# Kernel optimization log

Hardware: AMD Instinct MI355X
Metric: run time of the kernel (lower is better)

## Reference

```python
import math
import jax, jax.numpy as jnp
import numpy as np

MAX_CH = 21
D_CONV = 1024
LAT_DIM = 5
N_HEADS = 2            # TST_encoder hard-codes n_heads=2 (not PatchTSTEncoder's n_heads=8)
D_FF = 256
L_RAW = 38400
CONV_SPECS = [(512, 10, 5, 1), (512, 3, 2, 1), (512, 3, 2, 1), (1024, 3, 2, 1)]  # (dim,k,stride,dilation)
T_FRAMES = 959         # ((((38400-10)//5+1 -3)//2+1 -3)//2+1 -3)//2+1
T_TOTAL = MAX_CH * T_FRAMES  # 20139
L_LAT = MAX_CH * LAT_DIM     # 105


def sinusoid_table(n, d):
    pos = jnp.arange(n, dtype=jnp.float32)[:, None]
    div = jnp.exp(jnp.arange(0, d, 2, dtype=jnp.float32) * (-math.log(10000.0) / d))
    pe = jnp.zeros((n, d), jnp.float32)
    pe = pe.at[:, 0::2].set(jnp.sin(pos * div))
    pe = pe.at[:, 1::2].set(jnp.cos(pos * div))
    return pe


def setup_inputs() -> dict:
    key = jax.random.key(0)
    ks = jax.random.split(key, 16)
    x = jax.random.normal(ks[0], (1, MAX_CH, L_RAW), dtype=jnp.float32)
    # per-channel validity mask: first 17 of 21 channels valid, broadcast over frames
    ch_valid = jnp.arange(MAX_CH) < 17
    ch_mask = jnp.repeat(ch_valid, T_FRAMES)[None, None, :]  # (1,1,T_TOTAL) bool

    conv_params = {}
    in_c = 1
    for i, (dim, k, s, dil) in enumerate(CONV_SPECS):
        std = 1.0 / math.sqrt(in_c * k)
        conv_params[f"conv_w{i+1}"] = jax.random.normal(ks[1 + i], (dim, in_c, k), jnp.float32) * std
        conv_params[f"conv_b{i+1}"] = jnp.zeros((dim,), jnp.float32)
        in_c = dim

    ch_emb = sinusoid_table(MAX_CH, D_CONV)  # trainable channel embedding, sinusoidal init
    latent_q = jax.random.normal(ks[6], (L_LAT, D_CONV), jnp.float32) * math.sqrt(2.0 / (L_LAT + D_CONV))
    std_d = 1.0 / math.sqrt(D_CONV)
    wk_w = jax.random.normal(ks[7], (D_CONV, D_CONV), jnp.float32) * std_d
    wk_b = jnp.zeros((D_CONV,), jnp.float32)
    wv_w = jax.random.normal(ks[8], (D_CONV, D_CONV), jnp.float32) * std_d
    wv_b = jnp.zeros((D_CONV,), jnp.float32)
    ff_w1 = jax.random.normal(ks[9], (D_FF, D_CONV), jnp.float32) * std_d   # Linear(d_conv->d_ff), no bias
    ff_w2 = jax.random.normal(ks[10], (D_CONV, D_FF), jnp.float32) * (1.0 / math.sqrt(D_FF))
    return dict(x=x,
                conv_w1=conv_params["conv_w1"], conv_b1=conv_params["conv_b1"],
                conv_w2=conv_params["conv_w2"], conv_b2=conv_params["conv_b2"],
                conv_w3=conv_params["conv_w3"], conv_b3=conv_params["conv_b3"],
                conv_w4=conv_params["conv_w4"], conv_b4=conv_params["conv_b4"],
                ch_emb=ch_emb, latent_q=latent_q,
                wk_w=wk_w, wk_b=wk_b, wv_w=wv_w, wv_b=wv_b,
                ff_w1=ff_w1, ff_w2=ff_w2, ch_mask=ch_mask)


def _conv1d(x, w, b, stride, dilation):
    # x: (N, C_in, L), w: (C_out, C_in, K)
    y = jax.lax.conv_general_dilated(x, w, window_strides=(stride,), padding='VALID',
                                     rhs_dilation=(dilation,),
                                     dimension_numbers=('NCH', 'OIH', 'NCH'))
    return y + b[None, :, None]


def reference(x, conv_w1, conv_b1, conv_w2, conv_b2, conv_w3, conv_b3, conv_w4, conv_b4,
              ch_emb, latent_q, wk_w, wk_b, wv_w, wv_b, ff_w1, ff_w2, ch_mask):
    b, c_in, L = x.shape
    # --- ConvFeatureExtraction: per-channel conv stack (dropout is identity at eval) ---
    h = x.reshape(b * c_in, 1, L)
    weights = [(conv_w1, conv_b1), (conv_w2, conv_b2), (conv_w3, conv_b3), (conv_w4, conv_b4)]
    for (w, bi), (_, k, s, dil) in zip(weights, CONV_SPECS):
        h = jax.nn.gelu(_conv1d(h, w, bi, s, dil), approximate=False)
    t = h.shape[-1]
    x_conv = h.reshape(b, c_in, D_CONV, t).transpose(0, 1, 3, 2)  # (b, c_in, t, d_conv)

    # --- DataEmbedding: temporal sinusoid (buffer) + channel embedding (param) ---
    pe = sinusoid_table(t, D_CONV)                                # (t, d_conv)
    x_pos = x_conv + pe[None, None] + ch_emb[None, :, None, :]
    u = x_pos.reshape(b, c_in * t, D_CONV)                        # (1, T, d_conv)

    # --- perceiver_resampler (pre_norm=False: no LayerNorms applied) ---
    T = u.shape[1]
    d_h = D_CONV // N_HEADS
    lq = latent_q.reshape(1, N_HEADS, L_LAT, d_h)                 # exact torch .view semantics
    kproj = (u @ wk_w.T + wk_b).reshape(b, T, N_HEADS, d_h)
    vproj = (u @ wv_w.T + wv_b).reshape(b, T, N_HEADS, d_h)
    k = kproj.transpose(0, 2, 3, 1)                               # (b, H, d, T)
    v = vproj.transpose(0, 2, 1, 3)                               # (b, H, T, d)
    scale = N_HEADS ** (-0.5)                                     # note: heads, not d_k
    scores = jnp.einsum('bhld,bhdt->bhlt', lq, k) * scale         # (b, H, L_lat, T)
    mask = ch_mask[:, None, :, :]                                 # (b,1,1,T) -> broadcast
    scores = jnp.where(mask, scores, -1000000000.0)
    attn = jax.nn.softmax(scores, axis=-1)
    attn = jnp.where(mask, attn, 0.0)
    o = jnp.einsum('bhlt,bhtd->bhld', attn, v)                    # (b, H, L_lat, d)
    o = o.transpose(0, 2, 1, 3).reshape(b, L_LAT, D_CONV)

    # --- GELU FFN (bias=False) + residual ---
    ffn = jax.nn.gelu(o @ ff_w1.T, approximate=False) @ ff_w2.T
    return o + ffn
```

## Files before the change

### kernel.cpp

```cpp
#include <hip/hip_runtime.h>
#include <math.h>


#define NCH 17
#define LRAW 38400
#define LC1 7679
#define LC2 3839
#define LC3 1919
#define LC4 959
#define XA1 3840
#define XA2 1920
#define XA3 960
#define DC 1024
#define TVALID (NCH * LC4)
#define TPAD 16320
#define LLAT 105
#define DH 512
#define ASTR 40
#define ESTR 132

typedef unsigned short u16;
typedef __attribute__((ext_vector_type(8))) short bf16x8;
typedef __attribute__((ext_vector_type(4))) float f32x4;

__device__ __forceinline__ float bf2f(u16 s) {
    union { unsigned int u; float f; } cv; cv.u = ((unsigned int)s) << 16; return cv.f;
}
__device__ __forceinline__ u16 f2bf(float f) {
    union { float f; unsigned int u; } cv; cv.f = f;
    unsigned int u = cv.u;
    u += 0x7FFFu + ((u >> 16) & 1u);
    return (u16)(u >> 16);
}
__device__ __forceinline__ float gelu_exact(float x) {
    return 0.5f * x * (1.0f + erff(x * 0.70710678118654752f));
}
__device__ __forceinline__ float gelu_fast(float x) {
    float u = 0.7978845608f * x * (1.0f + 0.044715f * x * x);
    u = fminf(fmaxf(u, -9.0f), 9.0f);
    float e = __expf(2.0f * u);
    return 0.5f * x * (1.0f + (e - 1.0f) / (e + 1.0f));
}

__device__ __forceinline__ void gload16(const u16* g, u16* l) {
    __builtin_amdgcn_global_load_lds(
        (const __attribute__((address_space(1))) void*)g,
        (__attribute__((address_space(3))) void*)l, 16, 0, 0);
}

__device__ __forceinline__ int xcd_logical(int d, int N) {
    int q = N >> 3, r = N & 7, x = d & 7, j = d >> 3;
    return (x < r ? x * (q + 1) : r * (q + 1) + (x - r) * q) + j;
}

#define STAGE_TILE(lds, src, row0, ld, k0)                                          \
    {                                                                               \
        int m_ = tid >> 2, c_ = tid & 3;                                            \
        gload16(&(src)[(size_t)((row0) + m_) * (ld) + (k0) + ((c_ ^ ((m_ >> 1) & 3)) << 3)], \
                &(lds)[m_ * 32 + c_ * 8]);                                          \
        int m2_ = m_ + 64;                                                          \
        gload16(&(src)[(size_t)((row0) + m2_) * (ld) + (k0) + ((c_ ^ ((m2_ >> 1) & 3)) << 3)], \
                &(lds)[m2_ * 32 + c_ * 8]);                                         \
    }

#define FRAG(lds, R) \
    (*reinterpret_cast<const bf16x8*>(&(lds)[(R) * 32 + ((l4 ^ (((R) >> 1) & 3)) << 3)]))

__global__ void __launch_bounds__(256) cvt_kernel(
        const float* __restrict__ in, u16* __restrict__ out, int n) {
    int i = blockIdx.x * 256 + threadIdx.x;
    if (i < n) out[i] = f2bf(in[i]);
}

__global__ void __launch_bounds__(256) wsplit_kernel(
        const float* __restrict__ w, u16* __restrict__ out, int dout) {
    int idx = blockIdx.x * 256 + threadIdx.x;
    if (idx >= dout * 1536) return;
    int d = idx / 1536, k = idx - d * 1536;
    int ci = k / 3, jj = k - ci * 3;
    out[((size_t)jj * dout + d) * 512 + ci] = f2bf(w[idx]);
}

__global__ void __launch_bounds__(256) lqcvt_kernel(
        const float* __restrict__ lq, u16* __restrict__ lqbf) {
    int idx = blockIdx.x * 256 + threadIdx.x;
    if (idx >= 2 * 128 * 512) return;
    int h = idx >> 16, rem = idx & 65535;
    int m = rem >> 9, k = rem & 511;
    lqbf[idx] = (m < LLAT) ? f2bf(lq[(size_t)h * LLAT * DH + m * DH + k]) : (u16)0;
}

__global__ void __launch_bounds__(256) pe_kernel(float* __restrict__ pe) {
    int idx = blockIdx.x * 256 + threadIdx.x;
    if (idx >= LC4 * 512) return;
    int t = idx / 512, i = idx - (idx / 512) * 512;
    float f = expf((-2.0f * (float)i) * (9.210340371976184f / 1024.0f));
    float ang = (float)t * f;
    pe[t * DC + 2 * i]     = sinf(ang);
    pe[t * DC + 2 * i + 1] = cosf(ang);
}

__global__ void __launch_bounds__(256) conv1_kernel(
        const float* __restrict__ x, const float* __restrict__ w1,
        const float* __restrict__ b1, u16* __restrict__ out, int g0) {
    __shared__ float xs[64 * 5 + 5];
    int cg = blockIdx.y;
    int c  = g0 + cg;
    int t0 = blockIdx.x * 64;
    int nseg = min(64, LC1 - t0);
    int xlen = nseg * 5 + 5;
    const float* xrow = x + (size_t)c * LRAW + t0 * 5;
    int tid = threadIdx.x;
    if (tid < xlen) xs[tid] = xrow[tid];
    if (tid + 256 < xlen) xs[tid + 256] = xrow[tid + 256];
    int d0 = tid * 2;
    float wr0[10], wr1[10];
    #pragma unroll
    for (int j = 0; j < 10; ++j) {
        wr0[j] = w1[d0 * 10 + j];
        wr1[j] = w1[(d0 + 1) * 10 + j];
    }
    float bb0 = b1[d0], bb1 = b1[d0 + 1];
    __syncthreads();
    u16* outc = out + (size_t)cg * 2 * XA1 * 512;
    for (int tt = 0; tt < nseg; ++tt) {
        float a0 = bb0, a1 = bb1;
        #pragma unroll
        for (int j = 0; j < 10; ++j) {
            float xv = xs[tt * 5 + j];
            a0 += wr0[j] * xv;
            a1 += wr1[j] * xv;
        }
        int t = t0 + tt;
        ushort2 wv;
        wv.x = f2bf(gelu_fast(a0));
        wv.y = f2bf(gelu_fast(a1));
        *reinterpret_cast<ushort2*>(
            &outc[((size_t)(t & 1) * XA1 + (t >> 1)) * 512 + d0]) = wv;
    }
}

template <int DOUT, int XIN, int XOUT, int LOUT, int EPI, int NNT, int NMT>
__global__ void __launch_bounds__(256, 4) conv_mfma(
        const u16* __restrict__ in, const u16* __restrict__ wsplit,
        const float* __restrict__ bias, u16* __restrict__ out,
        const float* __restrict__ pe, const float* __restrict__ chemb,
        int g0) {
    __shared__ __align__(16) u16 SH[128 * ESTR];
    u16* const Asb[2] = {SH, SH + 4096};
    u16* const Bsb[2] = {SH + 8192, SH + 12288};
    int L = xcd_logical(blockIdx.x, gridDim.x);
    int mt = L % NMT;
    int rest = L / NMT;
    int nt = rest % NNT;
    int cg = rest / NNT;
    int m0 = mt * 128, n0 = nt * 128;
    int tid = threadIdx.x, lane = tid & 63, wave = tid >> 6;
    int wm = (wave >> 1) * 64, wn = (wave & 1) * 64;
    int l15 = lane & 15, l4 = lane >> 4;
    const u16* bufc = in + (size_t)cg * 2 * XIN * 512;
    const u16* wjp[3] = {wsplit, wsplit + (size_t)DOUT * 512,
                         wsplit + 2 * (size_t)DOUT * 512};
    const u16* bjp[3] = {bufc, bufc + (size_t)XIN * 512, bufc + 512};
    f32x4 acc[4][4] = {};

#define C_STAGE(s, buf)                                   \
    {                                                     \
        int jj_ = (s) >> 4, kk_ = ((s) & 15) << 5;        \
        STAGE_TILE(Asb[buf], wjp[jj_], m0, 512, kk_);     \
        STAGE_TILE(Bsb[buf], bjp[jj_], n0, 512, kk_);     \
    }
#define C_COMPUTE(buf)                                                        \
    {                                                                         \
        bf16x8 af[4], bfr[4];                                                 \
        _Pragma("unroll")                                                     \
        for (int mi = 0; mi < 4; ++mi) af[mi]  = FRAG(Asb[buf], wm + mi * 16 + l15); \
        _Pragma("unroll")                                                     \
        for (int ni = 0; ni < 4; ++ni) bfr[ni] = FRAG(Bsb[buf], wn + ni * 16 + l15); \
        _Pragma("unroll")                                                     \
        for (int mi = 0; mi < 4; ++mi)                                        \
            _Pragma("unroll")                                                 \
            for (int ni = 0; ni < 4; ++ni)                                    \
                acc[mi][ni] = __builtin_amdgcn_mfma_f32_16x16x32_bf16(        \
                    af[mi], bfr[ni], acc[mi][ni], 0, 0, 0);                   \
    }

    C_STAGE(0, 0);
    __syncthreads();
    for (int s = 0; s < 48; s += 2) {
        C_STAGE(s + 1, 1);
        C_COMPUTE(0);
        __syncthreads();
        if (s + 2 < 48) C_STAGE(s + 2, 0);
        C_COMPUTE(1);
        __syncthreads();
    }
#undef C_STAGE
#undef C_COMPUTE

    #pragma unroll
    for (int mi = 0; mi < 4; ++mi) {
        int ml = wm + mi * 16 + l4 * 4;
        #pragma unroll
        for (int ni = 0; ni < 4; ++ni) {
            int nl = wn + ni * 16 + l15;
            ushort4 sv;
            sv.x = f2bf(acc[mi][ni][0]); sv.y = f2bf(acc[mi][ni][1]);
            sv.z = f2bf(acc[mi][ni][2]); sv.w = f2bf(acc[mi][ni][3]);
            *reinterpret_cast<ushort4*>(&SH[nl * ESTR + ml]) = sv;
        }
    }
    __syncthreads();
    int row = tid >> 1, half = tid & 1;
    int t = n0 + row;
    if (t < LOUT) {
        const u16* srow = &SH[row * ESTR + half * 64];
        int d0 = m0 + half * 64;
        if (EPI == 0) {
            u16* dst = out + ((size_t)cg * 2 + (t & 1)) * (size_t)XOUT * 512
                           + (size_t)(t >> 1) * 512 + d0;
            #pragma unroll
            for (int q = 0; q < 8; ++q) {
                bf16x8 sv = *reinterpret_cast<const bf16x8*>(&srow[q * 8]);
                bf16x8 ov;
                #pragma unroll
                for (int e = 0; e < 8; ++e)
                    ov[e] = (short)f2bf(gelu_fast(bf2f((u16)sv[e]) + bias[d0 + q * 8 + e]));
                *reinterpret_cast<bf16x8*>(&dst[q * 8]) = ov;
            }
        } else {
            int c = g0 + cg;
            u16* dst = out + ((size_t)c * LC4 + t) * DC + d0;
            const float* per = &pe[(size_t)t * DC + d0];
            const float* chr = &chemb[(size_t)c * DC + d0];
            #pragma unroll
            for (int q = 0; q < 8; ++q) {
                bf16x8 sv = *reinterpret_cast<const bf16x8*>(&srow[q * 8]);
                bf16x8 ov;
                #pragma unroll
                for (int e = 0; e < 8; ++e)
                    ov[e] = (short)f2bf(gelu_fast(bf2f((u16)sv[e]) + bias[d0 + q * 8 + e])
                                        + per[q * 8 + e] + chr[q * 8 + e]);
                *reinterpret_cast<bf16x8*>(&dst[q * 8]) = ov;
            }
        }
    }
}

__global__ void __launch_bounds__(256, 4) projkv_mfma(
        const u16* __restrict__ u, const u16* __restrict__ wkv,
        const float* __restrict__ kb, const float* __restrict__ vb,
        u16* __restrict__ K, u16* __restrict__ Vt) {
    __shared__ __align__(16) u16 SH[128 * ESTR];
    u16* const Asb[2] = {SH, SH + 4096};
    u16* const Bsb[2] = {SH + 8192, SH + 12288};
    int L = xcd_logical(blockIdx.x, gridDim.x);
    int nt = L & 15;
    int mt = L >> 4;
    int m0 = mt * 128, n0 = nt * 128;
    int tid = threadIdx.x, lane = tid & 63, wave = tid >> 6;
    int wm = (wave >> 1) * 64, wn = (wave & 1) * 64;
    int l15 = lane & 15, l4 = lane >> 4;
    f32x4 acc[4][4] = {};

#define P_STAGE(s, buf)                               \
    {                                                 \
        int kk_ = (s) << 5;                           \
        STAGE_TILE(Asb[buf], u,   m0, DC, kk_);       \
        STAGE_TILE(Bsb[buf], wkv, n0, DC, kk_);       \
    }
#define P_COMPUTE(buf)                                                        \
    {                                                                         \
        bf16x8 af[4], bfr[4];                                                 \
        _Pragma("unroll")                                                     \
        for (int mi = 0; mi < 4; ++mi) af[mi]  = FRAG(Asb[buf], wm + mi * 16 + l15); \
        _Pragma("unroll")                                                     \
        for (int ni = 0; ni < 4; ++ni) bfr[ni] = FRAG(Bsb[buf], wn + ni * 16 + l15); \
        _Pragma("unroll")                                                     \
        for (int mi = 0; mi < 4; ++mi)                                        \
            _Pragma("unroll")                                                 \
            for (int ni = 0; ni < 4; ++ni)                                    \
                acc[mi][ni] = __builtin_amdgcn_mfma_f32_16x16x32_bf16(        \
                    af[mi], bfr[ni], acc[mi][ni], 0, 0, 0);                   \
    }

    P_STAGE(0, 0);
    __syncthreads();
    for (int s = 0; s < 32; s += 2) {
        P_STAGE(s + 1, 1);
        P_COMPUTE(0);
        __syncthreads();
        if (s + 2 < 32) P_STAGE(s + 2, 0);
        P_COMPUTE(1);
        __syncthreads();
    }
#undef P_STAGE
#undef P_COMPUTE

    if (n0 < 1024) {
        #pragma unroll
        for (int mi = 0; mi < 4; ++mi) {
            int ml = wm + mi * 16 + l4 * 4;
            #pragma unroll
            for (int ni = 0; ni < 4; ++ni) {
                int nl = wn + ni * 16 + l15;
                #pragma unroll
                for (int r = 0; r < 4; ++r)
                    SH[(ml + r) * ESTR + nl] = f2bf(acc[mi][ni][r]);
            }
        }
        __syncthreads();
        int row = tid >> 1, half = tid & 1;
        int t = m0 + row;
        if (t < TVALID) {
            const u16* srow = &SH[row * ESTR + half * 64];
            int nn = n0 + half * 64;
            u16* dst = K + (size_t)t * DC + nn;
            #pragma unroll
            for (int q = 0; q < 8; ++q) {
                bf16x8 sv = *reinterpret_cast<const bf16x8*>(&srow[q * 8]);
                bf16x8 ov;
                #pragma unroll
                for (int e = 0; e < 8; ++e)
                    ov[e] = (short)f2bf(bf2f((u16)sv[e]) + kb[nn + q * 8 + e]);
                *reinterpret_cast<bf16x8*>(&dst[q * 8]) = ov;
            }
        }
    } else {
        #pragma unroll
        for (int mi = 0; mi < 4; ++mi) {
            int ml = wm + mi * 16 + l4 * 4;
            #pragma unroll
            for (int ni = 0; ni < 4; ++ni) {
                int nl = wn + ni * 16 + l15;
                ushort4 sv;
                sv.x = f2bf(acc[mi][ni][0]); sv.y = f2bf(acc[mi][ni][1]);
                sv.z = f2bf(acc[mi][ni][2]); sv.w = f2bf(acc[mi][ni][3]);
                *reinterpret_cast<ushort4*>(&SH[nl * ESTR + ml]) = sv;
            }
        }
        __syncthreads();
        int row = tid >> 1, half = tid & 1;
        int j = (n0 - 1024) + row;
        int tbase = m0 + half * 64;
        if (tbase < TPAD) {
            float bj = vb[j];
            const u16* srow = &SH[row * ESTR + half * 64];
            u16* dst = Vt + (size_t)j * TPAD + tbase;
            #pragma unroll
            for (int q = 0; q < 8; ++q) {
                bf16x8 sv = *reinterpret_cast<const bf16x8*>(&srow[q * 8]);
                bf16x8 ov;
                #pragma unroll
                for (int e = 0; e < 8; ++e)
                    ov[e] = (short)f2bf(bf2f((u16)sv[e]) + bj);
                *reinterpret_cast<bf16x8*>(&dst[q * 8]) = ov;
            }
        }
    }
}

__global__ void __launch_bounds__(256) scores_mfma(
        const u16* __restrict__ lqbf, const u16* __restrict__ K,
        float* __restrict__ sc) {
    __shared__ __align__(16) u16 As[128 * ASTR];
    __shared__ __align__(16) u16 Bs[128 * ASTR];
    int n0 = blockIdx.x * 128;
    int h  = blockIdx.y;
    int tid = threadIdx.x, lane = tid & 63, wave = tid >> 6;
    int wm = (wave >> 1) * 64, wn = (wave & 1) * 64;
    int l15 = lane & 15, l4 = lane >> 4;
    const u16* lqh = lqbf + (size_t)h * 128 * DH;
    f32x4 acc[4][4] = {};
    for (int k0 = 0; k0 < DH; k0 += 32) {
        #pragma unroll
        for (int p = 0; p < 2; ++p) {
            int f = tid + p * 256;
            int m = f >> 2, kb = f & 3;
            bf16x8 va = *reinterpret_cast<const bf16x8*>(
                &lqh[(size_t)m * DH + k0 + kb * 8]);
            *reinterpret_cast<bf16x8*>(&As[m * ASTR + kb * 8]) = va;
            int n = n0 + m;
            bf16x8 vb;
            if (n < TVALID)
                vb = *reinterpret_cast<const bf16x8*>(
                    &K[(size_t)n * DC + h * DH + k0 + kb * 8]);
            else
                #pragma unroll
                for (int j = 0; j < 8; ++j) vb[j] = 0;
            *reinterpret_cast<bf16x8*>(&Bs[m * ASTR + kb * 8]) = vb;
        }
        __syncthreads();
        bf16x8 af[4], bfr[4];
        #pragma unroll
        for (int mi = 0; mi < 4; ++mi)
            af[mi] = *reinterpret_cast<const bf16x8*>(
                &As[(wm + mi * 16 + l15) * ASTR + l4 * 8]);
        #pragma unroll
        for (int ni = 0; ni < 4; ++ni)
            bfr[ni] = *reinterpret_cast<const bf16x8*>(
                &Bs[(wn + ni * 16 + l15) * ASTR + l4 * 8]);
        #pragma unroll
        for (int mi = 0; mi < 4; ++mi)
            #pragma unroll
            for (int ni = 0; ni < 4; ++ni)
                acc[mi][ni] = __builtin_amdgcn_mfma_f32_16x16x32_bf16(
                    af[mi], bfr[ni], acc[mi][ni], 0, 0, 0);
        __syncthreads();
    }
    #pragma unroll
    for (int mi = 0; mi < 4; ++mi) {
        int mbase = wm + mi * 16 + l4 * 4;
        #pragma unroll
        for (int ni = 0; ni < 4; ++ni) {
            int t = n0 + wn + ni * 16 + l15;
            if (t >= TVALID) continue;
            #pragma unroll
            for (int r = 0; r < 4; ++r) {
                int m = mbase + r;
                if (m < LLAT)
                    sc[((size_t)h * LLAT + m) * TVALID + t] =
                        acc[mi][ni][r] * 0.70710678118654752f;
            }
        }
    }
}

__global__ void __launch_bounds__(256) softmax_bf16(
        const float* __restrict__ sc, u16* __restrict__ attnP) {
    int r = blockIdx.x;
    const float* row = sc + (size_t)r * TVALID;
    u16* orow = attnP + (size_t)r * TPAD;
    __shared__ float red[8];
    int tid = threadIdx.x;
    float m = -1e30f;
    for (int i = tid; i < TVALID; i += 256) m = fmaxf(m, row[i]);
    #pragma unroll
    for (int off = 32; off > 0; off >>= 1) m = fmaxf(m, __shfl_down(m, off, 64));
    if ((tid & 63) == 0) red[tid >> 6] = m;
    __syncthreads();
    m = fmaxf(fmaxf(red[0], red[1]), fmaxf(red[2], red[3]));
    float s = 0.f;
    for (int i = tid; i < TVALID; i += 256) s += expf(row[i] - m);
    #pragma unroll
    for (int off = 32; off > 0; off >>= 1) s += __shfl_down(s, off, 64);
    if ((tid & 63) == 0) red[4 + (tid >> 6)] = s;
    __syncthreads();
    s = red[4] + red[5] + red[6] + red[7];
    float inv = 1.0f / s;
    for (int i = tid; i < TPAD; i += 256)
        orow[i] = (i < TVALID) ? f2bf(expf(row[i] - m) * inv) : (u16)0;
}

__global__ void __launch_bounds__(256) pv_mfma(
        const u16* __restrict__ attnP, const u16* __restrict__ Vt,
        float* __restrict__ o) {
    __shared__ __align__(16) u16 As[128 * ASTR];
    __shared__ __align__(16) u16 Bs[128 * ASTR];
    int n0 = blockIdx.x * 128;
    int kc = blockIdx.y;
    int h  = blockIdx.z;
    int tid = threadIdx.x, lane = tid & 63, wave = tid >> 6;
    int wm = (wave >> 1) * 64, wn = (wave & 1) * 64;
    int l15 = lane & 15, l4 = lane >> 4;
    f32x4 acc[4][4] = {};
    for (int it = 0; it < 15; ++it) {
        int k0 = (kc * 15 + it) * 32;
        #pragma unroll
        for (int p = 0; p < 2; ++p) {
            int f = tid + p * 256;
            int m = f >> 2, kb = f & 3;
            bf16x8 va;
            if (m < LLAT)
                va = *reinterpret_cast<const bf16x8*>(
                    &attnP[((size_t)h * LLAT + m) * TPAD + k0 + kb * 8]);
            else
                #pragma unroll
                for (int j = 0; j < 8; ++j) va[j] = 0;
            *reinterpret_cast<bf16x8*>(&As[m * ASTR + kb * 8]) = va;
            bf16x8 vb = *reinterpret_cast<const bf16x8*>(
                &Vt[((size_t)h * DH + n0 + m) * TPAD + k0 + kb * 8]);
            *reinterpret_cast<bf16x8*>(&Bs[m * ASTR + kb * 8]) = vb;
        }
        __syncthreads();
        bf16x8 af[4], bfr[4];
        #pragma unroll
        for (int mi = 0; mi < 4; ++mi)
            af[mi] = *reinterpret_cast<const bf16x8*>(
                &As[(wm + mi * 16 + l15) * ASTR + l4 * 8]);
        #pragma unroll
        for (int ni = 0; ni < 4; ++ni)
            bfr[ni] = *reinterpret_cast<const bf16x8*>(
                &Bs[(wn + ni * 16 + l15) * ASTR + l4 * 8]);
        #pragma unroll
        for (int mi = 0; mi < 4; ++mi)
            #pragma unroll
            for (int ni = 0; ni < 4; ++ni)
                acc[mi][ni] = __builtin_amdgcn_mfma_f32_16x16x32_bf16(
                    af[mi], bfr[ni], acc[mi][ni], 0, 0, 0);
        __syncthreads();
    }
    #pragma unroll
    for (int mi = 0; mi < 4; ++mi) {
        int mbase = wm + mi * 16 + l4 * 4;
        #pragma unroll
        for (int ni = 0; ni < 4; ++ni) {
            int n = n0 + wn + ni * 16 + l15;
            #pragma unroll
            for (int r = 0; r < 4; ++r) {
                int m = mbase + r;
                if (m < LLAT)
                    atomicAdd(&o[(size_t)m * DC + h * DH + n], acc[mi][ni][r]);
            }
        }
    }
}

__global__ void __launch_bounds__(256) ffn1_kernel(
        const float* __restrict__ o, const float* __restrict__ w1,
        float* __restrict__ h1) {
    __shared__ float os[DC];
    int l = blockIdx.x;
    for (int i = threadIdx.x; i < DC; i += 256) os[i] = o[(size_t)l * DC + i];
    __syncthreads();
    int f = threadIdx.x;
    const float* wr = w1 + (size_t)f * DC;
    float acc = 0.f;
    for (int d = 0; d < DC; ++d) acc += os[d] * wr[d];
    h1[(size_t)l * 256 + f] = gelu_exact(acc);
}

__global__ void __launch_bounds__(256) ffn2_kernel(
        const float* __restrict__ o, const float* __restrict__ h1,
        const float* __restrict__ w2, float* __restrict__ out) {
    __shared__ float hs[256];
    int l = blockIdx.x;
    hs[threadIdx.x] = h1[(size_t)l * 256 + threadIdx.x];
    __syncthreads();
    for (int d = threadIdx.x; d < DC; d += 256) {
        const float* wr = w2 + (size_t)d * 256;
        float acc = 0.f;
        for (int f = 0; f < 256; ++f) acc += hs[f] * wr[f];
        out[(size_t)l * DC + d] = o[(size_t)l * DC + d] + acc;
    }
}

constexpr size_t OFF_PE  = 0;
constexpr size_t OFF_WB2 = 3928064;
constexpr size_t OFF_WB3 = 5500928;
constexpr size_t OFF_WB4 = 7073792;
constexpr size_t OFF_WKV = 10219520;
constexpr size_t OFF_STATIC_END = 14413888;
constexpr size_t B_U   = 14413888;
constexpr size_t B_S1  = 47968320;
constexpr size_t B_S2  = 118747200;
constexpr size_t B_K   = 47968320;
constexpr size_t B_VT  = 81522752;
constexpr size_t B_SC  = 114946112;
constexpr size_t B_AP  = 128640640;
constexpr size_t B_LQ  = 135495040;
constexpr size_t B_O   = 135757184;
constexpr size_t B_H   = 136187264;
constexpr size_t A_S1  = 14413888;
constexpr size_t A_S2  = 148107328;
constexpr size_t A_U   = A_S2;
constexpr size_t A_K   = 14413888;
constexpr size_t A_VT  = 47968320;
constexpr size_t A_SC  = 81391680;
constexpr size_t A_AP  = 95086208;
constexpr size_t A_LQ  = 101940608;
constexpr size_t A_O   = 102202752;
constexpr size_t A_H   = 102632832;
constexpr size_t A_NEED = 214954048;

extern "C" void kernel_launch(void* const* d_in, const int* in_sizes, int n_in,
                              void* d_out, int out_size, void* d_ws, size_t ws_size,
                              hipStream_t stream) {
    (void)in_sizes; (void)n_in; (void)out_size;
    const float* x     = (const float*)d_in[0];
    const float* w1    = (const float*)d_in[1];
    const float* b1    = (const float*)d_in[2];
    const float* w2    = (const float*)d_in[3];
    const float* b2    = (const float*)d_in[4];
    const float* w3    = (const float*)d_in[5];
    const float* b3    = (const float*)d_in[6];
    const float* w4    = (const float*)d_in[7];
    const float* b4    = (const float*)d_in[8];
    const float* chemb = (const float*)d_in[9];
    const float* latq  = (const float*)d_in[10];
    const float* wkw   = (const float*)d_in[11];
    const float* wkb   = (const float*)d_in[12];
    const float* wvw   = (const float*)d_in[13];
    const float* wvb   = (const float*)d_in[14];
    const float* fw1   = (const float*)d_in[15];
    const float* fw2   = (const float*)d_in[16];
    float* out = (float*)d_out;
    char*  ws  = (char*)d_ws;

    const bool big = (ws_size >= A_NEED);

    float* pe    = (float*)(ws + OFF_PE);
    u16*   w2s   = (u16*)(ws + OFF_WB2);
    u16*   w3s   = (u16*)(ws + OFF_WB3);
    u16*   w4s   = (u16*)(ws + OFF_WB4);
    u16*   wkv   = (u16*)(ws + OFF_WKV);
    u16*   s1    = (u16*)(ws + (big ? A_S1 : B_S1));
    u16*   s2    = (u16*)(ws + (big ? A_S2 : B_S2));
    u16*   ubuf  = (u16*)(ws + (big ? A_U  : B_U));
    u16*   Kbuf  = (u16*)(ws + (big ? A_K  : B_K));
    u16*   Vt    = (u16*)(ws + (big ? A_VT : B_VT));
    float* sc    = (float*)(ws + (big ? A_SC : B_SC));
    u16*   attnP = (u16*)(ws + (big ? A_AP : B_AP));
    u16*   lqbf  = (u16*)(ws + (big ? A_LQ : B_LQ));
    float* obuf  = (float*)(ws + (big ? A_O  : B_O));
    float* h1    = (float*)(ws + (big ? A_H  : B_H));

    wsplit_kernel<<<(512 * 1536 + 255) / 256, 256, 0, stream>>>(w2, w2s, 512);
    wsplit_kernel<<<(512 * 1536 + 255) / 256, 256, 0, stream>>>(w3, w3s, 512);
    wsplit_kernel<<<(1024 * 1536 + 255) / 256, 256, 0, stream>>>(w4, w4s, 1024);
    cvt_kernel<<<(DC * DC + 255) / 256, 256, 0, stream>>>(wkw, wkv, DC * DC);
    cvt_kernel<<<(DC * DC + 255) / 256, 256, 0, stream>>>(wvw, wkv + (size_t)1024 * DC, DC * DC);
    pe_kernel<<<(LC4 * 512 + 255) / 256, 256, 0, stream>>>(pe);

    const int gmax = big ? 17 : 9;
    for (int g0 = 0; g0 < NCH; g0 += gmax) {
        int G = (NCH - g0 < gmax) ? (NCH - g0) : gmax;
        conv1_kernel<<<dim3((LC1 + 63) / 64, G), 256, 0, stream>>>(x, w1, b1, s1, g0);
        conv_mfma<512, XA1, XA2, LC2, 0, 30, 4><<<30 * 4 * G, 256, 0, stream>>>(
            s1, w2s, b2, s2, nullptr, nullptr, g0);
        conv_mfma<512, XA2, XA3, LC3, 0, 15, 4><<<15 * 4 * G, 256, 0, stream>>>(
            s2, w3s, b3, s1, nullptr, nullptr, g0);
        conv_mfma<1024, XA3, 0, LC4, 1, 8, 8><<<8 * 8 * G, 256, 0, stream>>>(
            s1, w4s, b4, ubuf, pe, chemb, g0);
    }

    projkv_mfma<<<16 * 128, 256, 0, stream>>>(ubuf, wkv, wkb, wvb, Kbuf, Vt);

    lqcvt_kernel<<<(2 * 128 * 512 + 255) / 256, 256, 0, stream>>>(latq, lqbf);
    scores_mfma<<<dim3(128, 2), 256, 0, stream>>>(lqbf, Kbuf, sc);
    softmax_bf16<<<210, 256, 0, stream>>>(sc, attnP);
    hipMemsetAsync(obuf, 0, (size_t)LLAT * DC * sizeof(float), stream);
    pv_mfma<<<dim3(4, 34, 2), 256, 0, stream>>>(attnP, Vt, obuf);
    ffn1_kernel<<<LLAT, 256, 0, stream>>>(obuf, fw1, h1);
    ffn2_kernel<<<LLAT, 256, 0, stream>>>(obuf, h1, fw2, out);
}
```

Measured before the change: 635.3 us.

## Double-buffer attention GEMMs, merge weight-prep launches, fuse FFN, widen softmax

```diff
diff --git a/kernel.cpp b/kernel.cpp
--- a/kernel.cpp
+++ b/kernel.cpp
@@ -16,7 +16,6 @@
 #define TPAD 16320
 #define LLAT 105
 #define DH 512
-#define ASTR 40
 #define ESTR 132
 
 typedef unsigned short u16;
@@ -66,19 +65,27 @@
 #define FRAG(lds, R) \
     (*reinterpret_cast<const bf16x8*>(&(lds)[(R) * 32 + ((l4 ^ (((R) >> 1) & 3)) << 3)]))
 
-__global__ void __launch_bounds__(256) cvt_kernel(
-        const float* __restrict__ in, u16* __restrict__ out, int n) {
-    int i = blockIdx.x * 256 + threadIdx.x;
-    if (i < n) out[i] = f2bf(in[i]);
-}
-
-__global__ void __launch_bounds__(256) wsplit_kernel(
-        const float* __restrict__ w, u16* __restrict__ out, int dout) {
+__global__ void __launch_bounds__(256) wsplit_all(
+        const float* __restrict__ w2, const float* __restrict__ w3,
+        const float* __restrict__ w4, u16* __restrict__ w2s,
+        u16* __restrict__ w3s, u16* __restrict__ w4s) {
     int idx = blockIdx.x * 256 + threadIdx.x;
-    if (idx >= dout * 1536) return;
+    if (idx >= 2048 * 1536) return;
     int d = idx / 1536, k = idx - d * 1536;
     int ci = k / 3, jj = k - ci * 3;
-    out[((size_t)jj * dout + d) * 512 + ci] = f2bf(w[idx]);
+    const float* w; u16* ws; int dout, dl;
+    if (d < 512)       { w = w2; ws = w2s; dout = 512;  dl = d; }
+    else if (d < 1024) { w = w3; ws = w3s; dout = 512;  dl = d - 512; }
+    else               { w = w4; ws = w4s; dout = 1024; dl = d - 1024; }
+    ws[((size_t)jj * dout + dl) * 512 + ci] = f2bf(w[(size_t)dl * 1536 + k]);
+}
+
+__global__ void __launch_bounds__(256) cvtkv_kernel(
+        const float* __restrict__ wk, const float* __restrict__ wv,
+        u16* __restrict__ out) {
+    int i = blockIdx.x * 256 + threadIdx.x;
+    if (i >= 2 * DC * DC) return;
+    out[i] = f2bf(i < DC * DC ? wk[i] : wv[i - DC * DC]);
 }
 
 __global__ void __launch_bounds__(256) lqcvt_kernel(
@@ -360,52 +367,43 @@
     }
 }
 
-__global__ void __launch_bounds__(256) scores_mfma(
-        const u16* __restrict__ lqbf, const u16* __restrict__ K,
+__global__ void __launch_bounds__(256, 4) scores_mfma(
+        const u16* __restrict__ lqbf, const u16* __restrict__ Kb,
         float* __restrict__ sc) {
-    __shared__ __align__(16) u16 As[128 * ASTR];
-    __shared__ __align__(16) u16 Bs[128 * ASTR];
+    __shared__ __align__(16) u16 SH[16384];
+    u16* const Asb[2] = {SH, SH + 4096};
+    u16* const Bsb[2] = {SH + 8192, SH + 12288};
     int n0 = blockIdx.x * 128;
     int h  = blockIdx.y;
     int tid = threadIdx.x, lane = tid & 63, wave = tid >> 6;
     int wm = (wave >> 1) * 64, wn = (wave & 1) * 64;
     int l15 = lane & 15, l4 = lane >> 4;
-    const u16* lqh = lqbf + (size_t)h * 128 * DH;
+    const u16* asrc = lqbf + (size_t)h * 128 * DH;
+    const u16* bsrc = Kb + (size_t)h * DH;
     f32x4 acc[4][4] = {};
-    for (int k0 = 0; k0 < DH; k0 += 32) {
-        #pragma unroll
-        for (int p = 0; p < 2; ++p) {
-            int f = tid + p * 256;
-            int m = f >> 2, kb = f & 3;
-            bf16x8 va = *reinterpret_cast<const bf16x8*>(
-                &lqh[(size_t)m * DH + k0 + kb * 8]);
-            *reinterpret_cast<bf16x8*>(&As[m * ASTR + kb * 8]) = va;
-            int n = n0 + m;
-            bf16x8 vb;
-            if (n < TVALID)
-                vb = *reinterpret_cast<const bf16x8*>(
-                    &K[(size_t)n * DC + h * DH + k0 + kb * 8]);
-            else
+    STAGE_TILE(Asb[0], asrc, 0, DH, 0);
+    STAGE_TILE(Bsb[0], bsrc, n0, DC, 0);
+    __syncthreads();
+    for (int s = 0; s < 16; ++s) {
+        if (s + 1 < 16) {
+            STAGE_TILE(Asb[(s + 1) & 1], asrc, 0, DH, (s + 1) * 32);
+            STAGE_TILE(Bsb[(s + 1) & 1], bsrc, n0, DC, (s + 1) * 32);
+        }
+        {
+            u16* A_ = Asb[s & 1];
+            u16* B_ = Bsb[s & 1];
+            bf16x8 af[4], bfr[4];
+            #pragma unroll
+            for (int mi = 0; mi < 4; ++mi) af[mi]  = FRAG(A_, wm + mi * 16 + l15);
+            #pragma unroll
+            for (int ni = 0; ni < 4; ++ni) bfr[ni] = FRAG(B_, wn + ni * 16 + l15);
+            #pragma unroll
+            for (int mi = 0; mi < 4; ++mi)
                 #pragma unroll
-                for (int j = 0; j < 8; ++j) vb[j] = 0;
-            *reinterpret_cast<bf16x8*>(&Bs[m * ASTR + kb * 8]) = vb;
-        }
-        __syncthreads();
-        bf16x8 af[4], bfr[4];
-        #pragma unroll
-        for (int mi = 0; mi < 4; ++mi)
-            af[mi] = *reinterpret_cast<const bf16x8*>(
-                &As[(wm + mi * 16 + l15) * ASTR + l4 * 8]);
-        #pragma unroll
-        for (int ni = 0; ni < 4; ++ni)
-            bfr[ni] = *reinterpret_cast<const bf16x8*>(
-                &Bs[(wn + ni * 16 + l15) * ASTR + l4 * 8]);
-        #pragma unroll
-        for (int mi = 0; mi < 4; ++mi)
-            #pragma unroll
-            for (int ni = 0; ni < 4; ++ni)
-                acc[mi][ni] = __builtin_amdgcn_mfma_f32_16x16x32_bf16(
-                    af[mi], bfr[ni], acc[mi][ni], 0, 0, 0);
+                for (int ni = 0; ni < 4; ++ni)
+                    acc[mi][ni] = __builtin_amdgcn_mfma_f32_16x16x32_bf16(
+                        af[mi], bfr[ni], acc[mi][ni], 0, 0, 0);
+        }
         __syncthreads();
     }
     #pragma unroll
@@ -426,78 +424,76 @@
     }
 }
 
-__global__ void __launch_bounds__(256) softmax_bf16(
+__global__ void __launch_bounds__(1024) softmax_bf16(
         const float* __restrict__ sc, u16* __restrict__ attnP) {
     int r = blockIdx.x;
     const float* row = sc + (size_t)r * TVALID;
     u16* orow = attnP + (size_t)r * TPAD;
-    __shared__ float red[8];
+    __shared__ float redm[16], reds[16];
     int tid = threadIdx.x;
     float m = -1e30f;
-    for (int i = tid; i < TVALID; i += 256) m = fmaxf(m, row[i]);
+    for (int i = tid; i < TVALID; i += 1024) m = fmaxf(m, row[i]);
     #pragma unroll
     for (int off = 32; off > 0; off >>= 1) m = fmaxf(m, __shfl_down(m, off, 64));
-    if ((tid & 63) == 0) red[tid >> 6] = m;
-    __syncthreads();
-    m = fmaxf(fmaxf(red[0], red[1]), fmaxf(red[2], red[3]));
+    if ((tid & 63) == 0) redm[tid >> 6] = m;
+    __syncthreads();
+    m = redm[0];
+    #pragma unroll
+    for (int i = 1; i < 16; ++i) m = fmaxf(m, redm[i]);
     float s = 0.f;
-    for (int i = tid; i < TVALID; i += 256) s += expf(row[i] - m);
+    for (int i = tid; i < TVALID; i += 1024) s += __expf(row[i] - m);
     #pragma unroll
     for (int off = 32; off > 0; off >>= 1) s += __shfl_down(s, off, 64);
-    if ((tid & 63) == 0) red[4 + (tid >> 6)] = s;
-    __syncthreads();
-    s = red[4] + red[5] + red[6] + red[7];
+    if ((tid & 63) == 0) reds[tid >> 6] = s;
+    __syncthreads();
+    s = 0.f;
+    #pragma unroll
+    for (int i = 0; i < 16; ++i) s += reds[i];
     float inv = 1.0f / s;
-    for (int i = tid; i < TPAD; i += 256)
-        orow[i] = (i < TVALID) ? f2bf(expf(row[i] - m) * inv) : (u16)0;
-}
-
-__global__ void __launch_bounds__(256) pv_mfma(
+    for (int i = tid; i < TPAD; i += 1024)
+        orow[i] = (i < TVALID) ? f2bf(__expf(row[i] - m) * inv) : (u16)0;
+}
+
+__global__ void __launch_bounds__(256, 4) pv_mfma(
         const u16* __restrict__ attnP, const u16* __restrict__ Vt,
         float* __restrict__ o) {
-    __shared__ __align__(16) u16 As[128 * ASTR];
-    __shared__ __align__(16) u16 Bs[128 * ASTR];
+    __shared__ __align__(16) u16 SH[16384];
+    u16* const Asb[2] = {SH, SH + 4096};
+    u16* const Bsb[2] = {SH + 8192, SH + 12288};
     int n0 = blockIdx.x * 128;
     int kc = blockIdx.y;
     int h  = blockIdx.z;
     int tid = threadIdx.x, lane = tid & 63, wave = tid >> 6;
     int wm = (wave >> 1) * 64, wn = (wave & 1) * 64;
     int l15 = lane & 15, l4 = lane >> 4;
+    const u16* asrc = attnP + (size_t)h * LLAT * TPAD;
+    const u16* bsrc = Vt + (size_t)h * DH * TPAD;
     f32x4 acc[4][4] = {};
-    for (int it = 0; it < 15; ++it) {
-        int k0 = (kc * 15 + it) * 32;
-        #pragma unroll
-        for (int p = 0; p < 2; ++p) {
-            int f = tid + p * 256;
-            int m = f >> 2, kb = f & 3;
-            bf16x8 va;
-            if (m < LLAT)
-                va = *reinterpret_cast<const bf16x8*>(
-                    &attnP[((size_t)h * LLAT + m) * TPAD + k0 + kb * 8]);
-            else
+    int kbase = kc * 15 * 32;
+    STAGE_TILE(Asb[0], asrc, 0, TPAD, kbase);
+    STAGE_TILE(Bsb[0], bsrc, n0, TPAD, kbase);
+    __syncthreads();
+    for (int s = 0; s < 15; ++s) {
+        if (s + 1 < 15) {
+            int k1 = kbase + (s + 1) * 32;
+            STAGE_TILE(Asb[(s + 1) & 1], asrc, 0, TPAD, k1);
+            STAGE_TILE(Bsb[(s + 1) & 1], bsrc, n0, TPAD, k1);
+        }
+        {
+            u16* A_ = Asb[s & 1];
+            u16* B_ = Bsb[s & 1];
+            bf16x8 af[4], bfr[4];
+            #pragma unroll
+            for (int mi = 0; mi < 4; ++mi) af[mi]  = FRAG(A_, wm + mi * 16 + l15);
+            #pragma unroll
+            for (int ni = 0; ni < 4; ++ni) bfr[ni] = FRAG(B_, wn + ni * 16 + l15);
+            #pragma unroll
+            for (int mi = 0; mi < 4; ++mi)
                 #pragma unroll
-                for (int j = 0; j < 8; ++j) va[j] = 0;
-            *reinterpret_cast<bf16x8*>(&As[m * ASTR + kb * 8]) = va;
-            bf16x8 vb = *reinterpret_cast<const bf16x8*>(
-                &Vt[((size_t)h * DH + n0 + m) * TPAD + k0 + kb * 8]);
-            *reinterpret_cast<bf16x8*>(&Bs[m * ASTR + kb * 8]) = vb;
-        }
-        __syncthreads();
-        bf16x8 af[4], bfr[4];
-        #pragma unroll
-        for (int mi = 0; mi < 4; ++mi)
-            af[mi] = *reinterpret_cast<const bf16x8*>(
-                &As[(wm + mi * 16 + l15) * ASTR + l4 * 8]);
-        #pragma unroll
-        for (int ni = 0; ni < 4; ++ni)
-            bfr[ni] = *reinterpret_cast<const bf16x8*>(
-                &Bs[(wn + ni * 16 + l15) * ASTR + l4 * 8]);
-        #pragma unroll
-        for (int mi = 0; mi < 4; ++mi)
-            #pragma unroll
-            for (int ni = 0; ni < 4; ++ni)
-                acc[mi][ni] = __builtin_amdgcn_mfma_f32_16x16x32_bf16(
-                    af[mi], bfr[ni], acc[mi][ni], 0, 0, 0);
+                for (int ni = 0; ni < 4; ++ni)
+                    acc[mi][ni] = __builtin_amdgcn_mfma_f32_16x16x32_bf16(
+                        af[mi], bfr[ni], acc[mi][ni], 0, 0, 0);
+        }
         __syncthreads();
     }
     #pragma unroll
@@ -516,10 +512,11 @@
     }
 }
 
-__global__ void __launch_bounds__(256) ffn1_kernel(
+__global__ void __launch_bounds__(256) ffn_kernel(
         const float* __restrict__ o, const float* __restrict__ w1,
-        float* __restrict__ h1) {
+        const float* __restrict__ w2, float* __restrict__ out) {
     __shared__ float os[DC];
+    __shared__ float hs[256];
     int l = blockIdx.x;
     for (int i = threadIdx.x; i < DC; i += 256) os[i] = o[(size_t)l * DC + i];
     __syncthreads();
@@ -527,21 +524,14 @@
     const float* wr = w1 + (size_t)f * DC;
     float acc = 0.f;
     for (int d = 0; d < DC; ++d) acc += os[d] * wr[d];
-    h1[(size_t)l * 256 + f] = gelu_exact(acc);
-}
-
-__global__ void __launch_bounds__(256) ffn2_kernel(
-        const float* __restrict__ o, const float* __restrict__ h1,
-        const float* __restrict__ w2, float* __restrict__ out) {
-    __shared__ float hs[256];
-    int l = blockIdx.x;
-    hs[threadIdx.x] = h1[(size_t)l * 256 + threadIdx.x];
+    hs[f] = gelu_exact(acc);
     __syncthreads();
     for (int d = threadIdx.x; d < DC; d += 256) {
-        const float* wr = w2 + (size_t)d * 256;
-        float acc = 0.f;
-        for (int f = 0; f < 256; ++f) acc += hs[f] * wr[f];
-        out[(size_t)l * DC + d] = o[(size_t)l * DC + d] + acc;
+        const float* w2r = w2 + (size_t)d * 256;
+        float a = 0.f;
+        #pragma unroll 8
+        for (int ff = 0; ff < 256; ++ff) a += hs[ff] * w2r[ff];
+        out[(size_t)l * DC + d] = os[d] + a;
     }
 }
 
@@ -550,7 +540,6 @@
 constexpr size_t OFF_WB3 = 5500928;
 constexpr size_t OFF_WB4 = 7073792;
 constexpr size_t OFF_WKV = 10219520;
-constexpr size_t OFF_STATIC_END = 14413888;
 constexpr size_t B_U   = 14413888;
 constexpr size_t B_S1  = 47968320;
 constexpr size_t B_S2  = 118747200;
@@ -614,12 +603,10 @@
     u16*   lqbf  = (u16*)(ws + (big ? A_LQ : B_LQ));
     float* obuf  = (float*)(ws + (big ? A_O  : B_O));
     float* h1    = (float*)(ws + (big ? A_H  : B_H));
-
-    wsplit_kernel<<<(512 * 1536 + 255) / 256, 256, 0, stream>>>(w2, w2s, 512);
-    wsplit_kernel<<<(512 * 1536 + 255) / 256, 256, 0, stream>>>(w3, w3s, 512);
-    wsplit_kernel<<<(1024 * 1536 + 255) / 256, 256, 0, stream>>>(w4, w4s, 1024);
-    cvt_kernel<<<(DC * DC + 255) / 256, 256, 0, stream>>>(wkw, wkv, DC * DC);
-    cvt_kernel<<<(DC * DC + 255) / 256, 256, 0, stream>>>(wvw, wkv + (size_t)1024 * DC, DC * DC);
+    (void)h1;
+
+    wsplit_all<<<(2048 * 1536 + 255) / 256, 256, 0, stream>>>(w2, w3, w4, w2s, w3s, w4s);
+    cvtkv_kernel<<<(2 * DC * DC + 255) / 256, 256, 0, stream>>>(wkw, wvw, wkv);
     pe_kernel<<<(LC4 * 512 + 255) / 256, 256, 0, stream>>>(pe);
 
     const int gmax = big ? 17 : 9;
@@ -638,9 +625,8 @@
 
     lqcvt_kernel<<<(2 * 128 * 512 + 255) / 256, 256, 0, stream>>>(latq, lqbf);
     scores_mfma<<<dim3(128, 2), 256, 0, stream>>>(lqbf, Kbuf, sc);
-    softmax_bf16<<<210, 256, 0, stream>>>(sc, attnP);
+    softmax_bf16<<<210, 1024, 0, stream>>>(sc, attnP);
     hipMemsetAsync(obuf, 0, (size_t)LLAT * DC * sizeof(float), stream);
     pv_mfma<<<dim3(4, 34, 2), 256, 0, stream>>>(attnP, Vt, obuf);
-    ffn1_kernel<<<LLAT, 256, 0, stream>>>(obuf, fw1, h1);
-    ffn2_kernel<<<LLAT, 256, 0, stream>>>(obuf, h1, fw2, out);
-}
+    ffn_kernel<<<LLAT, 256, 0, stream>>>(obuf, fw1, fw2, out);
+}
```

New measurement: 592.7 us. 1.07x faster.
